# Performance work log

Measured on AMD Instinct MI355X. Metric: run time of the kernel, lower is better.

## Reference

```python
import jax, jax.numpy as jnp
import numpy as np

N, E, F, H, L, G, B = 50000, 800000, 128, 128, 3, 32, 1024
BN_EPS = 1e-5


def setup_inputs() -> dict:
    key = jax.random.key(0)
    ks = jax.random.split(key, 16)
    x = jax.random.normal(ks[0], (N, F), dtype=jnp.float32)
    edge_index = jax.random.randint(ks[1], (2, E), 0, N, dtype=jnp.int64)
    batch = jnp.sort(jax.random.randint(ks[2], (N,), 0, B, dtype=jnp.int64))
    global_features = jax.random.normal(ks[3], (B, G), dtype=jnp.float32)
    wl = jax.random.normal(ks[4], (L, H, H), dtype=jnp.float32) * 0.1
    wr = jax.random.normal(ks[5], (L, H, H), dtype=jnp.float32) * 0.1
    b = jax.random.normal(ks[6], (L, H), dtype=jnp.float32) * 0.1
    bn_gamma = jax.random.uniform(ks[7], (L, H), dtype=jnp.float32) + 0.5
    bn_beta = jax.random.normal(ks[8], (L, H), dtype=jnp.float32) * 0.1
    bn_mean = jax.random.normal(ks[9], (L, H), dtype=jnp.float32) * 0.1
    bn_var = jax.random.uniform(ks[10], (L, H), dtype=jnp.float32) + 0.5
    fc1_w = jax.random.normal(ks[11], (H + G, H // 2), dtype=jnp.float32) * 0.1
    fc1_b = jax.random.normal(ks[12], (H // 2,), dtype=jnp.float32) * 0.1
    fc2_w = jax.random.normal(ks[13], (H // 2, 1), dtype=jnp.float32) * 0.1
    fc2_b = jax.random.normal(ks[14], (1,), dtype=jnp.float32) * 0.1
    return dict(x=x, edge_index=edge_index, batch=batch, global_features=global_features,
                wl=wl, wr=wr, b=b, bn_gamma=bn_gamma, bn_beta=bn_beta,
                bn_mean=bn_mean, bn_var=bn_var, fc1_w=fc1_w, fc1_b=fc1_b,
                fc2_w=fc2_w, fc2_b=fc2_b, num_graphs=B)


def _segment_mean(vals, seg_ids, num_segments):
    s = jax.ops.segment_sum(vals, seg_ids, num_segments=num_segments)
    cnt = jax.ops.segment_sum(jnp.ones((vals.shape[0],), vals.dtype), seg_ids,
                              num_segments=num_segments)
    return jnp.where(cnt[:, None] > 0, s / jnp.maximum(cnt, 1.0)[:, None], 0.0)


def reference(x, edge_index, batch, global_features, wl, wr, b,
              bn_gamma, bn_beta, bn_mean, bn_var,
              fc1_w, fc1_b, fc2_w, fc2_b, num_graphs):
    src, dst = edge_index[0], edge_index[1]
    h = x
    for i in range(L):
        # SAGEConv (mean aggr): lin_l(mean_{j in N(i)} h_j) + lin_r(h_i)
        agg = _segment_mean(h[src], dst, h.shape[0])          # [N, H]
        h = agg @ wl[i] + b[i] + h @ wr[i]                    # [N, H]
        # BatchNorm1d (eval: running stats); dropout is identity in eval
        h = (h - bn_mean[i]) * (bn_gamma[i] / jnp.sqrt(bn_var[i] + BN_EPS)) + bn_beta[i]
        h = jax.nn.relu(h)
    pooled = _segment_mean(h, batch, num_graphs)              # [B, H]
    z = jnp.concatenate([pooled, global_features], axis=1)    # [B, H+G]
    z = jax.nn.relu(z @ fc1_w + fc1_b)
    return z @ fc2_w + fc2_b                                  # [B, 1]
```

## Files before the change

kernel.cpp:

```cpp
#include <hip/hip_runtime.h>

#define HH 128
#define GG 32
#define LL 3
#define BN_EPS 1e-5f

typedef unsigned short ushortT;
typedef unsigned int uintT;
typedef __attribute__((ext_vector_type(8))) short bf16x8;
typedef __attribute__((ext_vector_type(4))) float f32x4;

__device__ inline ushortT f2bf(float f) {
  uintT u = __float_as_uint(f);
  u += 0x7fff + ((u >> 16) & 1);
  return (ushortT)(u >> 16);
}
__device__ inline float bf2f(ushortT u) { return __uint_as_float(((uintT)u) << 16); }

__global__ __launch_bounds__(256) void k_degpack(const int* __restrict__ ei, int* __restrict__ deg,
                                                 uintT* __restrict__ packed, ushortT* __restrict__ rank, int E) {
  int e = blockIdx.x * 256 + threadIdx.x;
  if (e < E) {
    int d = ei[E + e];
    int s = ei[e];
    int r = atomicAdd(&deg[d], 1);
    packed[e] = ((uintT)d << 16) | (uintT)s;
    rank[e] = (ushortT)r;
  }
}

__global__ __launch_bounds__(256) void k_cast(const float* __restrict__ in, ushortT* __restrict__ outb, int total4) {
  int i = blockIdx.x * 256 + threadIdx.x;
  if (i < total4) {
    float4 v = *(const float4*)&in[(size_t)i * 4];
    ushort4 o;
    o.x = f2bf(v.x); o.y = f2bf(v.y); o.z = f2bf(v.z); o.w = f2bf(v.w);
    *(ushort4*)&outb[(size_t)i * 4] = o;
  }
}

__global__ __launch_bounds__(256) void k_gbounds(const int* __restrict__ batch, int* __restrict__ goff,
                                                 int N, int B) {
  int g = blockIdx.x * 256 + threadIdx.x;
  if (g > B) return;
  if (g == B) { goff[B] = N; return; }
  int lo = 0, hi = N;
  while (lo < hi) {
    int mid = (lo + hi) >> 1;
    if (batch[mid] < g) lo = mid + 1; else hi = mid;
  }
  goff[g] = lo;
}

__global__ __launch_bounds__(1024) void k_scan_blk(const int* __restrict__ in, int* __restrict__ out,
                                                   int* __restrict__ bsum, int n) {
  __shared__ int sd[1024];
  int tid = threadIdx.x;
  int i = blockIdx.x * 1024 + tid;
  int v = (i < n) ? in[i] : 0;
  sd[tid] = v;
  __syncthreads();
  for (int off = 1; off < 1024; off <<= 1) {
    int t = (tid >= off) ? sd[tid - off] : 0;
    __syncthreads();
    sd[tid] += t;
    __syncthreads();
  }
  if (i < n) out[i] = sd[tid] - v;
  if (tid == 1023) bsum[blockIdx.x] = sd[1023];
}

__global__ __launch_bounds__(1024) void k_scan_top(int* __restrict__ bsum, int nb) {
  __shared__ int sd[1024];
  int tid = threadIdx.x;
  int v = (tid < nb) ? bsum[tid] : 0;
  sd[tid] = v;
  __syncthreads();
  for (int off = 1; off < 1024; off <<= 1) {
    int t = (tid >= off) ? sd[tid - off] : 0;
    __syncthreads();
    sd[tid] += t;
    __syncthreads();
  }
  if (tid < nb) bsum[tid] = sd[tid] - v;
}

__global__ __launch_bounds__(1024) void k_scan_add(int* __restrict__ out0, const int* __restrict__ bsum, int n) {
  int i = blockIdx.x * 1024 + threadIdx.x;
  if (i < n) out0[i] += bsum[blockIdx.x];
}

__global__ __launch_bounds__(256) void k_scatter(const uintT* __restrict__ packed, const ushortT* __restrict__ rank,
                                                 const int* __restrict__ csr_off, ushortT* __restrict__ csr_us, int E) {
  int e = blockIdx.x * 256 + threadIdx.x;
  if (e < E) {
    uintT p = packed[e];
    int d = (int)(p >> 16);
    int pos = csr_off[d] + (int)rank[e];
    csr_us[pos] = (ushortT)(p & 0xffffu);
  }
}

__global__ __launch_bounds__(256) void k_prepw(const float* __restrict__ wl, const float* __restrict__ wr,
                                               ushortT* __restrict__ wpack) {
  int idx = blockIdx.x * 256 + threadIdx.x;
  if (idx >= LL * 8 * 128 * 4) return;
  int q = idx & 3;
  int n = (idx >> 2) & 127;
  int kf = (idx >> 9) & 7;
  int layer = idx >> 12;
  ushortT tmp[8];
#pragma unroll
  for (int j = 0; j < 8; j++) {
    int k = kf * 32 + q * 8 + j;
    float w = (k < HH) ? wl[(size_t)layer * HH * HH + k * HH + n]
                       : wr[(size_t)layer * HH * HH + (k - HH) * HH + n];
    tmp[j] = f2bf(w);
  }
  ushort4 a = {tmp[0], tmp[1], tmp[2], tmp[3]};
  ushort4 b = {tmp[4], tmp[5], tmp[6], tmp[7]};
  *(ushort4*)&wpack[(size_t)idx * 8] = a;
  *(ushort4*)&wpack[(size_t)idx * 8 + 4] = b;
}

__global__ __launch_bounds__(256) void k_aggregate(const int* __restrict__ csr_off, const int* __restrict__ deg,
                                                   const ushortT* __restrict__ csr_us, const ushortT* __restrict__ hinb,
                                                   ushortT* __restrict__ aggb, int N) {
  int wid = (blockIdx.x * 256 + threadIdx.x) >> 6;
  int lane = threadIdx.x & 63;
  if (wid >= N) return;
  int off = csr_off[wid];
  int d = deg[wid];
  int half = lane >> 5;
  int colq = (lane & 31) * 4;
  float ax = 0.f, ay = 0.f, az = 0.f, aw = 0.f;
  int j = 0;
  for (; j + 8 <= d; j += 8) {
    int s0 = csr_us[off + j + half];
    int s1 = csr_us[off + j + 2 + half];
    int s2 = csr_us[off + j + 4 + half];
    int s3 = csr_us[off + j + 6 + half];
    ushort4 v0 = *(const ushort4*)&hinb[(size_t)s0 * HH + colq];
    ushort4 v1 = *(const ushort4*)&hinb[(size_t)s1 * HH + colq];
    ushort4 v2 = *(const ushort4*)&hinb[(size_t)s2 * HH + colq];
    ushort4 v3 = *(const ushort4*)&hinb[(size_t)s3 * HH + colq];
    ax += bf2f(v0.x); ay += bf2f(v0.y); az += bf2f(v0.z); aw += bf2f(v0.w);
    ax += bf2f(v1.x); ay += bf2f(v1.y); az += bf2f(v1.z); aw += bf2f(v1.w);
    ax += bf2f(v2.x); ay += bf2f(v2.y); az += bf2f(v2.z); aw += bf2f(v2.w);
    ax += bf2f(v3.x); ay += bf2f(v3.y); az += bf2f(v3.z); aw += bf2f(v3.w);
  }
  for (; j + 2 <= d; j += 2) {
    int s = csr_us[off + j + half];
    ushort4 v = *(const ushort4*)&hinb[(size_t)s * HH + colq];
    ax += bf2f(v.x); ay += bf2f(v.y); az += bf2f(v.z); aw += bf2f(v.w);
  }
  if (j < d && half == 0) {
    int s = csr_us[off + j];
    ushort4 v = *(const ushort4*)&hinb[(size_t)s * HH + colq];
    ax += bf2f(v.x); ay += bf2f(v.y); az += bf2f(v.z); aw += bf2f(v.w);
  }
  ax += __shfl_down(ax, 32);
  ay += __shfl_down(ay, 32);
  az += __shfl_down(az, 32);
  aw += __shfl_down(aw, 32);
  if (half == 0) {
    float inv = d > 0 ? 1.0f / (float)d : 0.0f;
    ushort4 o;
    o.x = f2bf(ax * inv); o.y = f2bf(ay * inv); o.z = f2bf(az * inv); o.w = f2bf(aw * inv);
    *(ushort4*)&aggb[(size_t)wid * HH + colq] = o;
  }
}

__global__ __launch_bounds__(256) void k_gemm(const ushortT* __restrict__ aggb, const ushortT* __restrict__ hinb,
                                              const ushortT* __restrict__ wpack, const float* __restrict__ bias,
                                              const float* __restrict__ gma, const float* __restrict__ bta,
                                              const float* __restrict__ mea, const float* __restrict__ var,
                                              ushortT* __restrict__ houtb, int N) {
  __shared__ char Asm[64 * 512];
  int tid = threadIdx.x;
  int l = tid & 63;
  int w = tid >> 6;
  int n0 = blockIdx.x * 64;
  int q = l >> 4;
  int ln = l & 15;

  bf16x8 bfr[8][2];
#pragma unroll
  for (int kf = 0; kf < 8; kf++)
#pragma unroll
    for (int nf = 0; nf < 2; nf++) {
      size_t off = (((size_t)kf * 128 + (w * 32 + nf * 16 + ln)) * 4 + q) * 8;
      bfr[kf][nf] = *(const bf16x8*)(wpack + off);
    }

#pragma unroll
  for (int r2 = 0; r2 < 8; r2++) {
    int c = r2 * 256 + tid;
    int row = c >> 5;
    int col16 = c & 31;
    int rg = n0 + row;
    rg = rg < N ? rg : N - 1;
    const ushortT* src = (col16 < 16) ? (aggb + (size_t)rg * HH + col16 * 8)
                                      : (hinb + (size_t)rg * HH + (col16 - 16) * 8);
    float4 v = *(const float4*)src;
    int waddr = row * 512 + ((col16 * 16) ^ ((row & 7) << 4));
    *(float4*)(Asm + waddr) = v;
  }
  __syncthreads();

  f32x4 acc[4][2] = {};
#pragma unroll
  for (int kf = 0; kf < 8; kf++) {
#pragma unroll
    for (int rt = 0; rt < 4; rt++) {
      int row = rt * 16 + ln;
      int raddr = row * 512 + ((kf * 64 + q * 16) ^ ((row & 7) << 4));
      bf16x8 a = *(const bf16x8*)(Asm + raddr);
      acc[rt][0] = __builtin_amdgcn_mfma_f32_16x16x32_bf16(a, bfr[kf][0], acc[rt][0], 0, 0, 0);
      acc[rt][1] = __builtin_amdgcn_mfma_f32_16x16x32_bf16(a, bfr[kf][1], acc[rt][1], 0, 0, 0);
    }
  }

  float sc[2], sh[2];
  int colg[2];
#pragma unroll
  for (int nf = 0; nf < 2; nf++) {
    int c = w * 32 + nf * 16 + ln;
    colg[nf] = c;
    float g = gma[c], vv = var[c], m = mea[c], bt = bta[c], bb = bias[c];
    float s = g * rsqrtf(vv + BN_EPS);
    sc[nf] = s;
    sh[nf] = (bb - m) * s + bt;
  }
#pragma unroll
  for (int rt = 0; rt < 4; rt++)
#pragma unroll
    for (int j = 0; j < 4; j++) {
      int row = n0 + rt * 16 + q * 4 + j;
      if (row < N) {
#pragma unroll
        for (int nf = 0; nf < 2; nf++) {
          float v = fmaxf(acc[rt][nf][j] * sc[nf] + sh[nf], 0.f);
          houtb[(size_t)row * HH + colg[nf]] = f2bf(v);
        }
      }
    }
}

__global__ __launch_bounds__(128) void k_poolmlp(const ushortT* __restrict__ hb, const int* __restrict__ goff,
                                                 const float* __restrict__ gfeat,
                                                 const float* __restrict__ w1, const float* __restrict__ b1,
                                                 const float* __restrict__ w2, const float* __restrict__ b2,
                                                 float* __restrict__ out) {
  __shared__ float z[HH + GG];
  int g = blockIdx.x;
  int t = threadIdx.x;
  int off = goff[g];
  int cnt = goff[g + 1] - off;
  float s = 0.f;
  int j = 0;
  for (; j + 2 <= cnt; j += 2)
    s += bf2f(hb[(size_t)(off + j) * HH + t]) + bf2f(hb[(size_t)(off + j + 1) * HH + t]);
  if (j < cnt) s += bf2f(hb[(size_t)(off + j) * HH + t]);
  z[t] = s * (cnt > 0 ? 1.0f / (float)cnt : 0.f);
  if (t < GG) z[HH + t] = gfeat[g * GG + t];
  __syncthreads();
  if (t < 64) {
    float acc = b1[t];
#pragma unroll 8
    for (int k = 0; k < HH + GG; k++) acc = fmaf(z[k], w1[k * 64 + t], acc);
    acc = fmaxf(acc, 0.f) * w2[t];
#pragma unroll
    for (int o = 32; o > 0; o >>= 1) acc += __shfl_down(acc, o);
    if (t == 0) out[g] = acc + b2[0];
  }
}

extern "C" void kernel_launch(void* const* d_in, const int* in_sizes, int n_in,
                              void* d_out, int out_size, void* d_ws, size_t ws_size,
                              hipStream_t stream) {
  const float* x = (const float*)d_in[0];
  const int* ei = (const int*)d_in[1];
  const int* batch = (const int*)d_in[2];
  const float* gfeat = (const float*)d_in[3];
  const float* wl = (const float*)d_in[4];
  const float* wr = (const float*)d_in[5];
  const float* bias = (const float*)d_in[6];
  const float* gma = (const float*)d_in[7];
  const float* bta = (const float*)d_in[8];
  const float* mea = (const float*)d_in[9];
  const float* var = (const float*)d_in[10];
  const float* w1 = (const float*)d_in[11];
  const float* b1 = (const float*)d_in[12];
  const float* w2 = (const float*)d_in[13];
  const float* b2 = (const float*)d_in[14];
  int N = in_sizes[0] / HH;
  int E = in_sizes[1] / 2;
  int B = in_sizes[3] / GG;
  float* out = (float*)d_out;
  (void)n_in; (void)out_size; (void)ws_size;

  char* base = (char*)d_ws;
  size_t off = 0;
  auto alloc = [&](size_t bytes) -> void* {
    void* p = base + off;
    off = (off + bytes + 255) & ~(size_t)255;
    return p;
  };
  int* deg = (int*)alloc((size_t)N * 4);
  int* csr_off = (int*)alloc((size_t)N * 4);
  int* goff = (int*)alloc((size_t)(B + 1) * 4);
  uintT* packed = (uintT*)alloc((size_t)E * 4);
  ushortT* rank = (ushortT*)alloc((size_t)E * 2);
  ushortT* csr_us = (ushortT*)alloc((size_t)E * 2);
  ushortT* xb = (ushortT*)alloc((size_t)N * HH * 2);
  ushortT* h1b = (ushortT*)alloc((size_t)N * HH * 2);
  ushortT* h2b = (ushortT*)alloc((size_t)N * HH * 2);
  ushortT* aggb = (ushortT*)alloc((size_t)N * HH * 2);
  ushortT* wpack = (ushortT*)alloc((size_t)LL * 8 * 128 * 4 * 8 * 2);
  int* bsumN = (int*)alloc(1024 * 4);

  hipMemsetAsync(deg, 0, (size_t)N * 4, stream);

  k_degpack<<<(E + 255) / 256, 256, 0, stream>>>(ei, deg, packed, rank, E);
  int total4 = N * HH / 4;
  k_cast<<<(total4 + 255) / 256, 256, 0, stream>>>(x, xb, total4);
  k_gbounds<<<(B + 256) / 256, 256, 0, stream>>>(batch, goff, N, B);

  int nbN = (N + 1023) / 1024;
  k_scan_blk<<<nbN, 1024, 0, stream>>>(deg, csr_off, bsumN, N);
  k_scan_top<<<1, 1024, 0, stream>>>(bsumN, nbN);
  k_scan_add<<<nbN, 1024, 0, stream>>>(csr_off, bsumN, N);

  k_scatter<<<(E + 255) / 256, 256, 0, stream>>>(packed, rank, csr_off, csr_us, E);

  k_prepw<<<(LL * 8 * 128 * 4 + 255) / 256, 256, 0, stream>>>(wl, wr, wpack);

  int nblk = (N + 63) / 64;
  int agg_blk = (N + 3) / 4;
  const ushortT* hsrc[LL] = {xb, h1b, h2b};
  ushortT* hdst[LL] = {h1b, h2b, h1b};
  for (int lyr = 0; lyr < LL; lyr++) {
    k_aggregate<<<agg_blk, 256, 0, stream>>>(csr_off, deg, csr_us, hsrc[lyr], aggb, N);
    k_gemm<<<nblk, 256, 0, stream>>>(aggb, hsrc[lyr], wpack + (size_t)lyr * 32768,
                                     bias + (size_t)lyr * HH, gma + (size_t)lyr * HH, bta + (size_t)lyr * HH,
                                     mea + (size_t)lyr * HH, var + (size_t)lyr * HH, hdst[lyr], N);
  }
  k_poolmlp<<<B, 128, 0, stream>>>(h1b, goff, gfeat, w1, b1, w2, b2, out);
}
```

Measured before the change: 221.8 us.

## Build CSR with windowed destination atomics instead of packed rank arrays

Replaces the degree-plus-rank pass and the rank-based scatter with two windowed passes. Each of eight block groups handles only the destinations in its own slice of N, so atomics stay localized (presumably per XCD or per cache region). The scatter now takes positions from an atomic cursor initialized from the scan, which removes the packed and rank intermediate arrays. The cost is that every group rereads the whole edge index, eight times the index traffic, and neighbor order within a row becomes nondeterministic.

```diff
diff --git a/kernel.cpp b/kernel.cpp
--- a/kernel.cpp
+++ b/kernel.cpp
@@ -17,15 +17,30 @@
 }
 __device__ inline float bf2f(ushortT u) { return __uint_as_float(((uintT)u) << 16); }
 
-__global__ __launch_bounds__(256) void k_degpack(const int* __restrict__ ei, int* __restrict__ deg,
-                                                 uintT* __restrict__ packed, ushortT* __restrict__ rank, int E) {
-  int e = blockIdx.x * 256 + threadIdx.x;
-  if (e < E) {
+__global__ __launch_bounds__(256) void k_degw(const int* __restrict__ ei, int* __restrict__ deg,
+                                              int E, int win) {
+  int w = blockIdx.x & 7;
+  int lo = w * win, hi = lo + win;
+  int idx = (blockIdx.x >> 3) * 256 + threadIdx.x;
+  int stride = (gridDim.x >> 3) * 256;
+  for (int e = idx; e < E; e += stride) {
     int d = ei[E + e];
-    int s = ei[e];
-    int r = atomicAdd(&deg[d], 1);
-    packed[e] = ((uintT)d << 16) | (uintT)s;
-    rank[e] = (ushortT)r;
+    if (d >= lo && d < hi) atomicAdd(&deg[d], 1);
+  }
+}
+
+__global__ __launch_bounds__(256) void k_scatw(const int* __restrict__ ei, int* __restrict__ cursor,
+                                               ushortT* __restrict__ csr_us, int E, int win) {
+  int w = blockIdx.x & 7;
+  int lo = w * win, hi = lo + win;
+  int idx = (blockIdx.x >> 3) * 256 + threadIdx.x;
+  int stride = (gridDim.x >> 3) * 256;
+  for (int e = idx; e < E; e += stride) {
+    int d = ei[E + e];
+    if (d >= lo && d < hi) {
+      int pos = atomicAdd(&cursor[d], 1);
+      csr_us[pos] = (ushortT)ei[e];
+    }
   }
 }
 
@@ -85,19 +100,13 @@
   if (tid < nb) bsum[tid] = sd[tid] - v;
 }
 
-__global__ __launch_bounds__(1024) void k_scan_add(int* __restrict__ out0, const int* __restrict__ bsum, int n) {
+__global__ __launch_bounds__(1024) void k_scan_add(int* __restrict__ out0, int* __restrict__ out1,
+                                                   const int* __restrict__ bsum, int n) {
   int i = blockIdx.x * 1024 + threadIdx.x;
-  if (i < n) out0[i] += bsum[blockIdx.x];
-}
-
-__global__ __launch_bounds__(256) void k_scatter(const uintT* __restrict__ packed, const ushortT* __restrict__ rank,
-                                                 const int* __restrict__ csr_off, ushortT* __restrict__ csr_us, int E) {
-  int e = blockIdx.x * 256 + threadIdx.x;
-  if (e < E) {
-    uintT p = packed[e];
-    int d = (int)(p >> 16);
-    int pos = csr_off[d] + (int)rank[e];
-    csr_us[pos] = (ushortT)(p & 0xffffu);
+  if (i < n) {
+    int v = out0[i] + bsum[blockIdx.x];
+    out0[i] = v;
+    out1[i] = v;
   }
 }
 
@@ -309,9 +318,8 @@
   };
   int* deg = (int*)alloc((size_t)N * 4);
   int* csr_off = (int*)alloc((size_t)N * 4);
+  int* cursor = (int*)alloc((size_t)N * 4);
   int* goff = (int*)alloc((size_t)(B + 1) * 4);
-  uintT* packed = (uintT*)alloc((size_t)E * 4);
-  ushortT* rank = (ushortT*)alloc((size_t)E * 2);
   ushortT* csr_us = (ushortT*)alloc((size_t)E * 2);
   ushortT* xb = (ushortT*)alloc((size_t)N * HH * 2);
   ushortT* h1b = (ushortT*)alloc((size_t)N * HH * 2);
@@ -322,7 +330,8 @@
 
   hipMemsetAsync(deg, 0, (size_t)N * 4, stream);
 
-  k_degpack<<<(E + 255) / 256, 256, 0, stream>>>(ei, deg, packed, rank, E);
+  int win = (N + 7) / 8;
+  k_degw<<<2048, 256, 0, stream>>>(ei, deg, E, win);
   int total4 = N * HH / 4;
   k_cast<<<(total4 + 255) / 256, 256, 0, stream>>>(x, xb, total4);
   k_gbounds<<<(B + 256) / 256, 256, 0, stream>>>(batch, goff, N, B);
@@ -330,9 +339,9 @@
   int nbN = (N + 1023) / 1024;
   k_scan_blk<<<nbN, 1024, 0, stream>>>(deg, csr_off, bsumN, N);
   k_scan_top<<<1, 1024, 0, stream>>>(bsumN, nbN);
-  k_scan_add<<<nbN, 1024, 0, stream>>>(csr_off, bsumN, N);
-
-  k_scatter<<<(E + 255) / 256, 256, 0, stream>>>(packed, rank, csr_off, csr_us, E);
+  k_scan_add<<<nbN, 1024, 0, stream>>>(csr_off, cursor, bsumN, N);
+
+  k_scatw<<<2048, 256, 0, stream>>>(ei, cursor, csr_us, E, win);
 
   k_prepw<<<(LL * 8 * 128 * 4 + 255) / 256, 256, 0, stream>>>(wl, wr, wpack);
 
```

Measured after the change: 249.7 us. 1.13x slower.

## Widen aggregate gathers to 16-byte rows and merge prep kernels into one

Applied to the files above, without the earlier changes.

The neighbor aggregation now splits each wavefront into four 16-lane groups. Each lane loads 8 bf16 values (16 bytes) per neighbor row, and the partial sums are combined with xor shuffles. This replaces the earlier 8-byte loads and two-way split, aiming for wider memory transactions and fewer loop-control instructions on the gather-bound path. Separately, the x cast, graph-boundary search and weight-packing kernels are fused into one launch to cut launch overhead. The new layout handles only four neighbors in flight per iteration, with an unroll of 4, and uses more accumulator registers.

```diff
diff --git a/kernel.cpp b/kernel.cpp
--- a/kernel.cpp
+++ b/kernel.cpp
@@ -8,6 +8,7 @@
 typedef unsigned short ushortT;
 typedef unsigned int uintT;
 typedef __attribute__((ext_vector_type(8))) short bf16x8;
+typedef __attribute__((ext_vector_type(8))) unsigned short us8;
 typedef __attribute__((ext_vector_type(4))) float f32x4;
 
 __device__ inline ushortT f2bf(float f) {
@@ -29,27 +30,46 @@
   }
 }
 
-__global__ __launch_bounds__(256) void k_cast(const float* __restrict__ in, ushortT* __restrict__ outb, int total4) {
+__global__ __launch_bounds__(256) void k_prep2(const float* __restrict__ x, ushortT* __restrict__ xb, int total4,
+                                               const int* __restrict__ batch, int* __restrict__ goff, int N, int B,
+                                               const float* __restrict__ wl, const float* __restrict__ wr,
+                                               ushortT* __restrict__ wpack) {
   int i = blockIdx.x * 256 + threadIdx.x;
   if (i < total4) {
-    float4 v = *(const float4*)&in[(size_t)i * 4];
+    float4 v = *(const float4*)&x[(size_t)i * 4];
     ushort4 o;
     o.x = f2bf(v.x); o.y = f2bf(v.y); o.z = f2bf(v.z); o.w = f2bf(v.w);
-    *(ushort4*)&outb[(size_t)i * 4] = o;
-  }
-}
-
-__global__ __launch_bounds__(256) void k_gbounds(const int* __restrict__ batch, int* __restrict__ goff,
-                                                 int N, int B) {
-  int g = blockIdx.x * 256 + threadIdx.x;
-  if (g > B) return;
-  if (g == B) { goff[B] = N; return; }
-  int lo = 0, hi = N;
-  while (lo < hi) {
-    int mid = (lo + hi) >> 1;
-    if (batch[mid] < g) lo = mid + 1; else hi = mid;
-  }
-  goff[g] = lo;
+    *(ushort4*)&xb[(size_t)i * 4] = o;
+  }
+  if (i <= B) {
+    if (i == B) goff[B] = N;
+    else {
+      int lo = 0, hi = N;
+      while (lo < hi) {
+        int mid = (lo + hi) >> 1;
+        if (batch[mid] < i) lo = mid + 1; else hi = mid;
+      }
+      goff[i] = lo;
+    }
+  }
+  if (i < LL * 8 * 128 * 4) {
+    int q = i & 3;
+    int n = (i >> 2) & 127;
+    int kf = (i >> 9) & 7;
+    int layer = i >> 12;
+    ushortT tmp[8];
+#pragma unroll
+    for (int j = 0; j < 8; j++) {
+      int k = kf * 32 + q * 8 + j;
+      float w = (k < HH) ? wl[(size_t)layer * HH * HH + k * HH + n]
+                         : wr[(size_t)layer * HH * HH + (k - HH) * HH + n];
+      tmp[j] = f2bf(w);
+    }
+    ushort4 a = {tmp[0], tmp[1], tmp[2], tmp[3]};
+    ushort4 b = {tmp[4], tmp[5], tmp[6], tmp[7]};
+    *(ushort4*)&wpack[(size_t)i * 8] = a;
+    *(ushort4*)&wpack[(size_t)i * 8 + 4] = b;
+  }
 }
 
 __global__ __launch_bounds__(1024) void k_scan_blk(const int* __restrict__ in, int* __restrict__ out,
@@ -101,28 +121,6 @@
   }
 }
 
-__global__ __launch_bounds__(256) void k_prepw(const float* __restrict__ wl, const float* __restrict__ wr,
-                                               ushortT* __restrict__ wpack) {
-  int idx = blockIdx.x * 256 + threadIdx.x;
-  if (idx >= LL * 8 * 128 * 4) return;
-  int q = idx & 3;
-  int n = (idx >> 2) & 127;
-  int kf = (idx >> 9) & 7;
-  int layer = idx >> 12;
-  ushortT tmp[8];
-#pragma unroll
-  for (int j = 0; j < 8; j++) {
-    int k = kf * 32 + q * 8 + j;
-    float w = (k < HH) ? wl[(size_t)layer * HH * HH + k * HH + n]
-                       : wr[(size_t)layer * HH * HH + (k - HH) * HH + n];
-    tmp[j] = f2bf(w);
-  }
-  ushort4 a = {tmp[0], tmp[1], tmp[2], tmp[3]};
-  ushort4 b = {tmp[4], tmp[5], tmp[6], tmp[7]};
-  *(ushort4*)&wpack[(size_t)idx * 8] = a;
-  *(ushort4*)&wpack[(size_t)idx * 8 + 4] = b;
-}
-
 __global__ __launch_bounds__(256) void k_aggregate(const int* __restrict__ csr_off, const int* __restrict__ deg,
                                                    const ushortT* __restrict__ csr_us, const ushortT* __restrict__ hinb,
                                                    ushortT* __restrict__ aggb, int N) {
@@ -131,43 +129,29 @@
   if (wid >= N) return;
   int off = csr_off[wid];
   int d = deg[wid];
-  int half = lane >> 5;
-  int colq = (lane & 31) * 4;
-  float ax = 0.f, ay = 0.f, az = 0.f, aw = 0.f;
-  int j = 0;
-  for (; j + 8 <= d; j += 8) {
-    int s0 = csr_us[off + j + half];
-    int s1 = csr_us[off + j + 2 + half];
-    int s2 = csr_us[off + j + 4 + half];
-    int s3 = csr_us[off + j + 6 + half];
-    ushort4 v0 = *(const ushort4*)&hinb[(size_t)s0 * HH + colq];
-    ushort4 v1 = *(const ushort4*)&hinb[(size_t)s1 * HH + colq];
-    ushort4 v2 = *(const ushort4*)&hinb[(size_t)s2 * HH + colq];
-    ushort4 v3 = *(const ushort4*)&hinb[(size_t)s3 * HH + colq];
-    ax += bf2f(v0.x); ay += bf2f(v0.y); az += bf2f(v0.z); aw += bf2f(v0.w);
-    ax += bf2f(v1.x); ay += bf2f(v1.y); az += bf2f(v1.z); aw += bf2f(v1.w);
-    ax += bf2f(v2.x); ay += bf2f(v2.y); az += bf2f(v2.z); aw += bf2f(v2.w);
-    ax += bf2f(v3.x); ay += bf2f(v3.y); az += bf2f(v3.z); aw += bf2f(v3.w);
-  }
-  for (; j + 2 <= d; j += 2) {
-    int s = csr_us[off + j + half];
-    ushort4 v = *(const ushort4*)&hinb[(size_t)s * HH + colq];
-    ax += bf2f(v.x); ay += bf2f(v.y); az += bf2f(v.z); aw += bf2f(v.w);
-  }
-  if (j < d && half == 0) {
+  int qrt = lane >> 4;
+  int li = lane & 15;
+  float acc[8] = {};
+#pragma unroll 4
+  for (int j = qrt; j < d; j += 4) {
     int s = csr_us[off + j];
-    ushort4 v = *(const ushort4*)&hinb[(size_t)s * HH + colq];
-    ax += bf2f(v.x); ay += bf2f(v.y); az += bf2f(v.z); aw += bf2f(v.w);
-  }
-  ax += __shfl_down(ax, 32);
-  ay += __shfl_down(ay, 32);
-  az += __shfl_down(az, 32);
-  aw += __shfl_down(aw, 32);
-  if (half == 0) {
+    us8 v = *(const us8*)&hinb[(size_t)s * HH + li * 8];
+#pragma unroll
+    for (int k = 0; k < 8; k++) acc[k] += bf2f(v[k]);
+  }
+#pragma unroll
+  for (int k = 0; k < 8; k++) {
+    acc[k] += __shfl_xor(acc[k], 16);
+    acc[k] += __shfl_xor(acc[k], 32);
+  }
+  if (lane < 16) {
     float inv = d > 0 ? 1.0f / (float)d : 0.0f;
-    ushort4 o;
-    o.x = f2bf(ax * inv); o.y = f2bf(ay * inv); o.z = f2bf(az * inv); o.w = f2bf(aw * inv);
-    *(ushort4*)&aggb[(size_t)wid * HH + colq] = o;
+    uint4 o;
+    o.x = (uintT)f2bf(acc[0] * inv) | ((uintT)f2bf(acc[1] * inv) << 16);
+    o.y = (uintT)f2bf(acc[2] * inv) | ((uintT)f2bf(acc[3] * inv) << 16);
+    o.z = (uintT)f2bf(acc[4] * inv) | ((uintT)f2bf(acc[5] * inv) << 16);
+    o.w = (uintT)f2bf(acc[6] * inv) | ((uintT)f2bf(acc[7] * inv) << 16);
+    *(uint4*)&aggb[(size_t)wid * HH + li * 8] = o;
   }
 }
 
@@ -323,9 +307,9 @@
   hipMemsetAsync(deg, 0, (size_t)N * 4, stream);
 
   k_degpack<<<(E + 255) / 256, 256, 0, stream>>>(ei, deg, packed, rank, E);
+
   int total4 = N * HH / 4;
-  k_cast<<<(total4 + 255) / 256, 256, 0, stream>>>(x, xb, total4);
-  k_gbounds<<<(B + 256) / 256, 256, 0, stream>>>(batch, goff, N, B);
+  k_prep2<<<(total4 + 255) / 256, 256, 0, stream>>>(x, xb, total4, batch, goff, N, B, wl, wr, wpack);
 
   int nbN = (N + 1023) / 1024;
   k_scan_blk<<<nbN, 1024, 0, stream>>>(deg, csr_off, bsumN, N);
@@ -333,8 +317,6 @@
   k_scan_add<<<nbN, 1024, 0, stream>>>(csr_off, bsumN, N);
 
   k_scatter<<<(E + 255) / 256, 256, 0, stream>>>(packed, rank, csr_off, csr_us, E);
-
-  k_prepw<<<(LL * 8 * 128 * 4 + 255) / 256, 256, 0, stream>>>(wl, wr, wpack);
 
   int nblk = (N + 63) / 64;
   int agg_blk = (N + 3) / 4;
```

Result: faster. 214.5 us (-3.3%).
